# Optimization experiments

Hardware: AMD Instinct MI355X
Metric: run time of the kernel (lower is better)

## Reference

```python
import jax, jax.numpy as jnp
import numpy as np

N_INP = 10
N_REC = 200
ALPHA = 0.1          # dt / tau = 0.01 / 0.1
NOISE_STD = 0.01
W_REC_SCALE = 0.5
W_INP_SCALE = 0.1
BATCH = 256
T = 1000


def setup_inputs() -> dict:
    key = jax.random.key(0)
    kx, kwi, kwr = jax.random.split(key, 3)
    x = jax.random.normal(kx, (BATCH, T, N_INP), dtype=jnp.float32)
    h0 = jnp.zeros((BATCH, N_REC), dtype=jnp.float32)
    W_inp = (W_INP_SCALE / np.sqrt(N_INP)) * jax.random.normal(kwi, (N_REC, N_INP), dtype=jnp.float32)
    W_rec = (W_REC_SCALE / np.sqrt(N_REC)) * jax.random.normal(kwr, (N_REC, N_REC), dtype=jnp.float32)
    b_rec = jnp.zeros((N_REC,), dtype=jnp.float32)
    return {"x": x, "h0": h0, "W_inp": W_inp, "W_rec": W_rec, "b_rec": b_rec}


def reference(x, h0, W_inp, W_rec, b_rec):
    """Euler-discretized rate RNN: h' = h + alpha*(-h + tanh(W_rec h + W_inp x + b) + noise).
    Returns states: [batch, time, n_rec]."""
    B, Tlen, _ = x.shape
    # Precompute input drive for all timesteps in one GEMM: [B,T,n_rec]
    inp_term = jnp.einsum('bti,ri->btr', x, W_inp) + b_rec
    # Per-step noise, deterministic key (mirrors torch.randn_like each step)
    noise_key = jax.random.key(42)
    eta = NOISE_STD * jax.random.normal(noise_key, (Tlen, B, W_rec.shape[0]), dtype=x.dtype)

    def step(h, xs):
        inp_t, eta_t = xs
        preact = h @ W_rec.T + inp_t          # [B, n_rec]
        rate = jnp.tanh(preact)
        h_next = h + ALPHA * (-h + rate + eta_t)
        return h_next, h_next

    _, states = jax.lax.scan(step, h0, (jnp.swapaxes(inp_term, 0, 1), eta))
    return jnp.swapaxes(states, 0, 1)  # [B, T, n_rec]
```

## Files before the change

kernel.cpp:

```cpp
#include <hip/hip_runtime.h>
#include <cstdint>
#include <cstddef>

#define TSTEPS 1000
#define NB     256
#define NR     200
#define NI     10
#define ALPHA_F     0.1f
#define NOISE_STD_F 0.01f

__device__ __forceinline__ uint32_t rotl32(uint32_t v, uint32_t d) {
  return (v << d) | (v >> (32u - d));
}

__device__ __forceinline__ uint32_t threefry_bits(uint32_t c1) {
  const uint32_t ks0 = 0u;
  const uint32_t ks1 = 42u;
  const uint32_t ks2 = 0x1BD11BDAu ^ ks0 ^ ks1;
  uint32_t x0 = ks0;
  uint32_t x1 = c1 + ks1;
#define TFR(r) { x0 += x1; x1 = rotl32(x1, (r)); x1 ^= x0; }
  TFR(13) TFR(15) TFR(26) TFR(6)   x0 += ks1; x1 += ks2 + 1u;
  TFR(17) TFR(29) TFR(16) TFR(24)  x0 += ks2; x1 += ks0 + 2u;
  TFR(13) TFR(15) TFR(26) TFR(6)   x0 += ks0; x1 += ks1 + 3u;
  TFR(17) TFR(29) TFR(16) TFR(24)  x0 += ks1; x1 += ks2 + 4u;
  TFR(13) TFR(15) TFR(26) TFR(6)   x0 += ks2; x1 += ks0 + 5u;
#undef TFR
  return x0 ^ x1;
}

__device__ __forceinline__ float erfinv_f32(float x) {
  float w = -__logf(fmaf(-x, x, 1.0f));
  float p;
  if (w < 5.0f) {
    w = w - 2.5f;
    p = 2.81022636e-08f;
    p = fmaf(p, w, 3.43273939e-07f);
    p = fmaf(p, w, -3.5233877e-06f);
    p = fmaf(p, w, -4.39150654e-06f);
    p = fmaf(p, w, 0.00021858087f);
    p = fmaf(p, w, -0.00125372503f);
    p = fmaf(p, w, -0.00417768164f);
    p = fmaf(p, w, 0.246640727f);
    p = fmaf(p, w, 1.50140941f);
  } else {
    w = sqrtf(w) - 3.0f;
    p = -0.000200214257f;
    p = fmaf(p, w, 0.000100950558f);
    p = fmaf(p, w, 0.00134934322f);
    p = fmaf(p, w, -0.00367342844f);
    p = fmaf(p, w, 0.00573950773f);
    p = fmaf(p, w, -0.0076224613f);
    p = fmaf(p, w, 0.00943887047f);
    p = fmaf(p, w, 1.00167406f);
    p = fmaf(p, w, 2.83297682f);
  }
  return p * x;
}

__device__ __forceinline__ float jax_normal(uint32_t idx) {
  uint32_t bits = threefry_bits(idx);
  float f = __uint_as_float((bits >> 9) | 0x3F800000u) - 1.0f;
  const float lo = -0.99999994f;
  float u = fmaf(f, 2.0f, lo);
  u = fmaxf(lo, u);
  return 1.41421356f * erfinv_f32(u);
}

__device__ __forceinline__ float tanh_fast(float y) {
  float ay = fabsf(y);
  float t  = __expf(-2.0f * ay);
  float r  = (1.0f - t) * __frcp_rn(1.0f + t);
  return copysignf(r, y);
}

__device__ __forceinline__ void wg_barrier_lds() {
  asm volatile("s_waitcnt lgkmcnt(0)\n\ts_barrier" ::: "memory");
}

template <int CUR, bool PF>
__device__ __forceinline__ void rnn_step(
    int t, int tid, bool mac_active,
    const float (&w)[4][20], const float (&winp)[NI], float brec_r,
    float& h_reg, float*& obp, float& xnA, float& xnB,
    const float* __restrict__ xb, uint32_t nb_b,
    const float* __restrict__ hp, float* __restrict__ part_wp,
    float* __restrict__ sh_h, float* __restrict__ sh_part,
    float (*__restrict__ sh_x)[16], float (*__restrict__ sh_eta)[NR]) {
  constexpr int NXT = CUR ^ 1;

  if (mac_active) {
    float a0 = 0.0f, a1 = 0.0f, a2 = 0.0f, a3 = 0.0f;
#pragma unroll
    for (int q = 0; q < 5; ++q) {
      float4 hv = *(const float4*)(hp + 4 * q);
      a0 = fmaf(w[0][4 * q + 0], hv.x, a0);
      a1 = fmaf(w[1][4 * q + 0], hv.x, a1);
      a2 = fmaf(w[2][4 * q + 0], hv.x, a2);
      a3 = fmaf(w[3][4 * q + 0], hv.x, a3);
      a0 = fmaf(w[0][4 * q + 1], hv.y, a0);
      a1 = fmaf(w[1][4 * q + 1], hv.y, a1);
      a2 = fmaf(w[2][4 * q + 1], hv.y, a2);
      a3 = fmaf(w[3][4 * q + 1], hv.y, a3);
      a0 = fmaf(w[0][4 * q + 2], hv.z, a0);
      a1 = fmaf(w[1][4 * q + 2], hv.z, a1);
      a2 = fmaf(w[2][4 * q + 2], hv.z, a2);
      a3 = fmaf(w[3][4 * q + 2], hv.z, a3);
      a0 = fmaf(w[0][4 * q + 3], hv.w, a0);
      a1 = fmaf(w[1][4 * q + 3], hv.w, a1);
      a2 = fmaf(w[2][4 * q + 3], hv.w, a2);
      a3 = fmaf(w[3][4 * q + 3], hv.w, a3);
    }
    *(float4*)part_wp = make_float4(a0, a1, a2, a3);
  }
  wg_barrier_lds();

  if (tid < NR) {
    float y = brec_r;
#pragma unroll
    for (int q = 0; q < 10; ++q) y += sh_part[q * NR + tid];
    float4 xv0 = *(const float4*)(&sh_x[CUR][0]);
    float4 xv1 = *(const float4*)(&sh_x[CUR][4]);
    float2 xv2 = *(const float2*)(&sh_x[CUR][8]);
    y = fmaf(winp[0], xv0.x, y);
    y = fmaf(winp[1], xv0.y, y);
    y = fmaf(winp[2], xv0.z, y);
    y = fmaf(winp[3], xv0.w, y);
    y = fmaf(winp[4], xv1.x, y);
    y = fmaf(winp[5], xv1.y, y);
    y = fmaf(winp[6], xv1.z, y);
    y = fmaf(winp[7], xv1.w, y);
    y = fmaf(winp[8], xv2.x, y);
    y = fmaf(winp[9], xv2.y, y);
    float rate = tanh_fast(y);
    float eta  = sh_eta[CUR][tid];
    float hn = h_reg + ALPHA_F * (((-h_reg) + rate) + eta);
    h_reg = hn;
    sh_h[tid] = hn;
    *obp = hn;
    obp += NR;
  } else if ((tid >= 256 && tid < 448) || (tid < 208)) {
    if (PF) {
      int n = (tid >= 256) ? (tid - 256) : (tid - 8);
      uint32_t idx = (uint32_t)(t + 1) * (uint32_t)(NB * NR) + nb_b + (uint32_t)n;
      sh_eta[NXT][n] = NOISE_STD_F * jax_normal(idx);
    }
  } else if (tid >= 448 && tid < 448 + NI) {
    if (PF) {
      int j = tid - 448;
      sh_x[NXT][j] = (CUR == 0) ? xnA : xnB;
      int tf = t + 3;
      if (tf > TSTEPS - 1) tf = TSTEPS - 1;
      float xl = xb[tf * NI + j];
      if (CUR == 0) xnA = xl; else xnB = xl;
    }
  }
  wg_barrier_lds();
}

__launch_bounds__(512, 2)
__global__ void rnn_persistent(const float* __restrict__ x,
                               const float* __restrict__ h0,
                               const float* __restrict__ Winp,
                               const float* __restrict__ Wrec,
                               const float* __restrict__ brec,
                               float* __restrict__ out) {
  const int b   = blockIdx.x;
  const int tid = threadIdx.x;

  __shared__ float sh_h[NR];
  __shared__ float sh_part[10 * NR];
  __shared__ float sh_x[2][16];
  __shared__ float sh_eta[2][NR];

  const int  k_th = tid / 50;
  const int  r_th = tid % 50;
  const bool mac_active = (tid < 500);

  float w[4][20];
  if (mac_active) {
#pragma unroll
    for (int j = 0; j < 4; ++j) {
      const float* wr = Wrec + (size_t)(4 * r_th + j) * NR + 20 * k_th;
#pragma unroll
      for (int q = 0; q < 5; ++q) {
        float4 v = *(const float4*)(wr + 4 * q);
        w[j][4 * q + 0] = v.x; w[j][4 * q + 1] = v.y;
        w[j][4 * q + 2] = v.z; w[j][4 * q + 3] = v.w;
      }
    }
  }

  float winp[NI];
  float brec_r = 0.0f;
  float h_reg  = 0.0f;
  float* obp   = nullptr;

  const float* xb = x + (size_t)b * TSTEPS * NI;
  float* ob       = out + (size_t)b * TSTEPS * NR;

  if (tid < NR) {
#pragma unroll
    for (int i = 0; i < NI; ++i) winp[i] = Winp[tid * NI + i];
    brec_r = brec[tid];
    h_reg  = h0[(size_t)b * NR + tid];
    sh_h[tid] = h_reg;
    obp = ob + tid;
  }

  const uint32_t nb_b = (uint32_t)b * (uint32_t)NR;
  float xnA = 0.0f, xnB = 0.0f;

  if ((tid >= 256 && tid < 448) || (tid >= 200 && tid < 208)) {
    int n = (tid >= 256) ? (tid - 256) : (tid - 8);
    sh_eta[0][n] = NOISE_STD_F * jax_normal(nb_b + (uint32_t)n);
  } else if (tid >= 448 && tid < 448 + NI) {
    int j = tid - 448;
    sh_x[0][j] = xb[j];
    xnA = xb[NI + j];
    xnB = xb[2 * NI + j];
  }
  __syncthreads();

  const float* hp      = sh_h + 20 * k_th;
  float*       part_wp = sh_part + k_th * NR + 4 * r_th;

  for (int t = 0; t < TSTEPS - 2; t += 2) {
    rnn_step<0, true>(t,     tid, mac_active, w, winp, brec_r, h_reg, obp,
                      xnA, xnB, xb, nb_b, hp, part_wp,
                      sh_h, sh_part, sh_x, sh_eta);
    rnn_step<1, true>(t + 1, tid, mac_active, w, winp, brec_r, h_reg, obp,
                      xnA, xnB, xb, nb_b, hp, part_wp,
                      sh_h, sh_part, sh_x, sh_eta);
  }
  rnn_step<0, true >(TSTEPS - 2, tid, mac_active, w, winp, brec_r, h_reg, obp,
                     xnA, xnB, xb, nb_b, hp, part_wp,
                     sh_h, sh_part, sh_x, sh_eta);
  rnn_step<1, false>(TSTEPS - 1, tid, mac_active, w, winp, brec_r, h_reg, obp,
                     xnA, xnB, xb, nb_b, hp, part_wp,
                     sh_h, sh_part, sh_x, sh_eta);
}

extern "C" void kernel_launch(void* const* d_in, const int* in_sizes, int n_in,
                              void* d_out, int out_size, void* d_ws, size_t ws_size,
                              hipStream_t stream) {
  const float* x    = (const float*)d_in[0];
  const float* h0   = (const float*)d_in[1];
  const float* Winp = (const float*)d_in[2];
  const float* Wrec = (const float*)d_in[3];
  const float* brec = (const float*)d_in[4];
  float* out = (float*)d_out;
  (void)in_sizes; (void)n_in; (void)out_size; (void)d_ws; (void)ws_size;

  rnn_persistent<<<dim3(NB), dim3(512), 0, stream>>>(x, h0, Winp, Wrec, brec, out);
}
```

Baseline: 982.1 us.

## Give each thread a full W_rec row and use one barrier per step

Each of 200 active threads now keeps a whole W_rec row in registers and computes its dot product against a double-buffered shared h. This removes the cross-thread partial-sum reduction through shared memory and the second workgroup barrier in every timestep. Noise generation moves into the row threads and is held in registers one step ahead. The block shrinks to 256 threads. The trade-off is a longer serial FMA chain and RNG work per thread on the critical path, plus higher register pressure.

```diff
diff --git a/kernel.cpp b/kernel.cpp
--- a/kernel.cpp
+++ b/kernel.cpp
@@ -80,45 +80,53 @@
 
 template <int CUR, bool PF>
 __device__ __forceinline__ void rnn_step(
-    int t, int tid, bool mac_active,
-    const float (&w)[4][20], const float (&winp)[NI], float brec_r,
-    float& h_reg, float*& obp, float& xnA, float& xnB,
-    const float* __restrict__ xb, uint32_t nb_b,
-    const float* __restrict__ hp, float* __restrict__ part_wp,
-    float* __restrict__ sh_h, float* __restrict__ sh_part,
-    float (*__restrict__ sh_x)[16], float (*__restrict__ sh_eta)[NR]) {
+    int t, int row, bool row_active, bool xpipe, int jx,
+    const float (&w)[NR], const float (&winp)[NI], float brec_r,
+    float& h_reg, float& eta_use, float& eta_fill,
+    float& xnA, float& xnB, float*& obp,
+    const float* __restrict__ xb, uint32_t nbase,
+    float (&sh_h)[2][NR], float (&sh_x)[2][16]) {
   constexpr int NXT = CUR ^ 1;
 
-  if (mac_active) {
-    float a0 = 0.0f, a1 = 0.0f, a2 = 0.0f, a3 = 0.0f;
+  if (row_active) {
+    if (PF) {
+      uint32_t idx = (uint32_t)(t + 1) * (uint32_t)(NB * NR) + nbase;
+      eta_fill = NOISE_STD_F * jax_normal(idx);
+    }
+
+    float y = brec_r;
+    const float* hb = &sh_h[CUR][0];
 #pragma unroll
-    for (int q = 0; q < 5; ++q) {
-      float4 hv = *(const float4*)(hp + 4 * q);
-      a0 = fmaf(w[0][4 * q + 0], hv.x, a0);
-      a1 = fmaf(w[1][4 * q + 0], hv.x, a1);
-      a2 = fmaf(w[2][4 * q + 0], hv.x, a2);
-      a3 = fmaf(w[3][4 * q + 0], hv.x, a3);
-      a0 = fmaf(w[0][4 * q + 1], hv.y, a0);
-      a1 = fmaf(w[1][4 * q + 1], hv.y, a1);
-      a2 = fmaf(w[2][4 * q + 1], hv.y, a2);
-      a3 = fmaf(w[3][4 * q + 1], hv.y, a3);
-      a0 = fmaf(w[0][4 * q + 2], hv.z, a0);
-      a1 = fmaf(w[1][4 * q + 2], hv.z, a1);
-      a2 = fmaf(w[2][4 * q + 2], hv.z, a2);
-      a3 = fmaf(w[3][4 * q + 2], hv.z, a3);
-      a0 = fmaf(w[0][4 * q + 3], hv.w, a0);
-      a1 = fmaf(w[1][4 * q + 3], hv.w, a1);
-      a2 = fmaf(w[2][4 * q + 3], hv.w, a2);
-      a3 = fmaf(w[3][4 * q + 3], hv.w, a3);
-    }
-    *(float4*)part_wp = make_float4(a0, a1, a2, a3);
-  }
-  wg_barrier_lds();
-
-  if (tid < NR) {
-    float y = brec_r;
-#pragma unroll
-    for (int q = 0; q < 10; ++q) y += sh_part[q * NR + tid];
+    for (int q = 0; q < 10; ++q) {
+      float4 h0 = *(const float4*)(hb + 20 * q + 0);
+      float4 h1 = *(const float4*)(hb + 20 * q + 4);
+      float4 h2 = *(const float4*)(hb + 20 * q + 8);
+      float4 h3 = *(const float4*)(hb + 20 * q + 12);
+      float4 h4 = *(const float4*)(hb + 20 * q + 16);
+      float p = 0.0f;
+      p = fmaf(w[20 * q +  0], h0.x, p);
+      p = fmaf(w[20 * q +  1], h0.y, p);
+      p = fmaf(w[20 * q +  2], h0.z, p);
+      p = fmaf(w[20 * q +  3], h0.w, p);
+      p = fmaf(w[20 * q +  4], h1.x, p);
+      p = fmaf(w[20 * q +  5], h1.y, p);
+      p = fmaf(w[20 * q +  6], h1.z, p);
+      p = fmaf(w[20 * q +  7], h1.w, p);
+      p = fmaf(w[20 * q +  8], h2.x, p);
+      p = fmaf(w[20 * q +  9], h2.y, p);
+      p = fmaf(w[20 * q + 10], h2.z, p);
+      p = fmaf(w[20 * q + 11], h2.w, p);
+      p = fmaf(w[20 * q + 12], h3.x, p);
+      p = fmaf(w[20 * q + 13], h3.y, p);
+      p = fmaf(w[20 * q + 14], h3.z, p);
+      p = fmaf(w[20 * q + 15], h3.w, p);
+      p = fmaf(w[20 * q + 16], h4.x, p);
+      p = fmaf(w[20 * q + 17], h4.y, p);
+      p = fmaf(w[20 * q + 18], h4.z, p);
+      p = fmaf(w[20 * q + 19], h4.w, p);
+      y += p;
+    }
+
     float4 xv0 = *(const float4*)(&sh_x[CUR][0]);
     float4 xv1 = *(const float4*)(&sh_x[CUR][4]);
     float2 xv2 = *(const float2*)(&sh_x[CUR][8]);
@@ -132,33 +140,26 @@
     y = fmaf(winp[7], xv1.w, y);
     y = fmaf(winp[8], xv2.x, y);
     y = fmaf(winp[9], xv2.y, y);
+
     float rate = tanh_fast(y);
-    float eta  = sh_eta[CUR][tid];
-    float hn = h_reg + ALPHA_F * (((-h_reg) + rate) + eta);
+    float hn = h_reg + ALPHA_F * (((-h_reg) + rate) + eta_use);
     h_reg = hn;
-    sh_h[tid] = hn;
+    sh_h[NXT][row] = hn;
     *obp = hn;
     obp += NR;
-  } else if ((tid >= 256 && tid < 448) || (tid < 208)) {
+  } else if (xpipe) {
     if (PF) {
-      int n = (tid >= 256) ? (tid - 256) : (tid - 8);
-      uint32_t idx = (uint32_t)(t + 1) * (uint32_t)(NB * NR) + nb_b + (uint32_t)n;
-      sh_eta[NXT][n] = NOISE_STD_F * jax_normal(idx);
-    }
-  } else if (tid >= 448 && tid < 448 + NI) {
-    if (PF) {
-      int j = tid - 448;
-      sh_x[NXT][j] = (CUR == 0) ? xnA : xnB;
+      sh_x[NXT][jx] = (CUR == 0) ? xnA : xnB;
       int tf = t + 3;
       if (tf > TSTEPS - 1) tf = TSTEPS - 1;
-      float xl = xb[tf * NI + j];
+      float xl = xb[tf * NI + jx];
       if (CUR == 0) xnA = xl; else xnB = xl;
     }
   }
   wg_barrier_lds();
 }
 
-__launch_bounds__(512, 2)
+__launch_bounds__(256, 1)
 __global__ void rnn_persistent(const float* __restrict__ x,
                                const float* __restrict__ h0,
                                const float* __restrict__ Winp,
@@ -167,78 +168,66 @@
                                float* __restrict__ out) {
   const int b   = blockIdx.x;
   const int tid = threadIdx.x;
-
-  __shared__ float sh_h[NR];
-  __shared__ float sh_part[10 * NR];
+  const int wv  = tid >> 6;
+  const int ln  = tid & 63;
+
+  __shared__ float sh_h[2][NR];
   __shared__ float sh_x[2][16];
-  __shared__ float sh_eta[2][NR];
-
-  const int  k_th = tid / 50;
-  const int  r_th = tid % 50;
-  const bool mac_active = (tid < 500);
-
-  float w[4][20];
-  if (mac_active) {
-#pragma unroll
-    for (int j = 0; j < 4; ++j) {
-      const float* wr = Wrec + (size_t)(4 * r_th + j) * NR + 20 * k_th;
-#pragma unroll
-      for (int q = 0; q < 5; ++q) {
-        float4 v = *(const float4*)(wr + 4 * q);
-        w[j][4 * q + 0] = v.x; w[j][4 * q + 1] = v.y;
-        w[j][4 * q + 2] = v.z; w[j][4 * q + 3] = v.w;
-      }
-    }
-  }
-
+
+  const bool row_active = (ln < 50);
+  const int  row        = wv * 50 + ln;
+  const bool xpipe      = (tid >= 50 && tid < 50 + NI);
+  const int  jx         = tid - 50;
+
+  const float* xb = x + (size_t)b * TSTEPS * NI;
+  float* ob       = out + (size_t)b * TSTEPS * NR;
+
+  float w[NR];
   float winp[NI];
   float brec_r = 0.0f;
   float h_reg  = 0.0f;
-  float* obp   = nullptr;
-
-  const float* xb = x + (size_t)b * TSTEPS * NI;
-  float* ob       = out + (size_t)b * TSTEPS * NR;
-
-  if (tid < NR) {
+  float etaA = 0.0f, etaB = 0.0f;
+  float* obp = nullptr;
+  uint32_t nbase = 0;
+
+  if (row_active) {
+    const float* wr = Wrec + (size_t)row * NR;
 #pragma unroll
-    for (int i = 0; i < NI; ++i) winp[i] = Winp[tid * NI + i];
-    brec_r = brec[tid];
-    h_reg  = h0[(size_t)b * NR + tid];
-    sh_h[tid] = h_reg;
-    obp = ob + tid;
-  }
-
-  const uint32_t nb_b = (uint32_t)b * (uint32_t)NR;
+    for (int i = 0; i < 50; ++i) {
+      float4 v = *(const float4*)(wr + 4 * i);
+      w[4 * i + 0] = v.x; w[4 * i + 1] = v.y;
+      w[4 * i + 2] = v.z; w[4 * i + 3] = v.w;
+    }
+#pragma unroll
+    for (int i = 0; i < NI; ++i) winp[i] = Winp[row * NI + i];
+    brec_r = brec[row];
+    h_reg  = h0[(size_t)b * NR + row];
+    sh_h[0][row] = h_reg;
+    obp = ob + row;
+    nbase = (uint32_t)b * (uint32_t)NR + (uint32_t)row;
+    etaA = NOISE_STD_F * jax_normal(nbase);
+  } else if (xpipe) {
+    sh_x[0][jx] = xb[jx];
+    etaA = xb[NI + jx];
+    xnA_init:;
+  }
   float xnA = 0.0f, xnB = 0.0f;
-
-  if ((tid >= 256 && tid < 448) || (tid >= 200 && tid < 208)) {
-    int n = (tid >= 256) ? (tid - 256) : (tid - 8);
-    sh_eta[0][n] = NOISE_STD_F * jax_normal(nb_b + (uint32_t)n);
-  } else if (tid >= 448 && tid < 448 + NI) {
-    int j = tid - 448;
-    sh_x[0][j] = xb[j];
-    xnA = xb[NI + j];
-    xnB = xb[2 * NI + j];
+  if (xpipe) {
+    xnA = xb[NI + jx];
+    xnB = xb[2 * NI + jx];
   }
   __syncthreads();
 
-  const float* hp      = sh_h + 20 * k_th;
-  float*       part_wp = sh_part + k_th * NR + 4 * r_th;
-
   for (int t = 0; t < TSTEPS - 2; t += 2) {
-    rnn_step<0, true>(t,     tid, mac_active, w, winp, brec_r, h_reg, obp,
-                      xnA, xnB, xb, nb_b, hp, part_wp,
-                      sh_h, sh_part, sh_x, sh_eta);
-    rnn_step<1, true>(t + 1, tid, mac_active, w, winp, brec_r, h_reg, obp,
-                      xnA, xnB, xb, nb_b, hp, part_wp,
-                      sh_h, sh_part, sh_x, sh_eta);
-  }
-  rnn_step<0, true >(TSTEPS - 2, tid, mac_active, w, winp, brec_r, h_reg, obp,
-                     xnA, xnB, xb, nb_b, hp, part_wp,
-                     sh_h, sh_part, sh_x, sh_eta);
-  rnn_step<1, false>(TSTEPS - 1, tid, mac_active, w, winp, brec_r, h_reg, obp,
-                     xnA, xnB, xb, nb_b, hp, part_wp,
-                     sh_h, sh_part, sh_x, sh_eta);
+    rnn_step<0, true>(t,     row, row_active, xpipe, jx, w, winp, brec_r,
+                      h_reg, etaA, etaB, xnA, xnB, obp, xb, nbase, sh_h, sh_x);
+    rnn_step<1, true>(t + 1, row, row_active, xpipe, jx, w, winp, brec_r,
+                      h_reg, etaB, etaA, xnA, xnB, obp, xb, nbase, sh_h, sh_x);
+  }
+  rnn_step<0, true >(TSTEPS - 2, row, row_active, xpipe, jx, w, winp, brec_r,
+                     h_reg, etaA, etaB, xnA, xnB, obp, xb, nbase, sh_h, sh_x);
+  rnn_step<1, false>(TSTEPS - 1, row, row_active, xpipe, jx, w, winp, brec_r,
+                     h_reg, etaB, etaA, xnA, xnB, obp, xb, nbase, sh_h, sh_x);
 }
 
 extern "C" void kernel_launch(void* const* d_in, const int* in_sizes, int n_in,
@@ -252,5 +241,5 @@
   float* out = (float*)d_out;
   (void)in_sizes; (void)n_in; (void)out_size; (void)d_ws; (void)ws_size;
 
-  rnn_persistent<<<dim3(NB), dim3(512), 0, stream>>>(x, h0, Winp, Wrec, brec, out);
-}
+  rnn_persistent<<<dim3(NB), dim3(256), 0, stream>>>(x, h0, Winp, Wrec, brec, out);
+}
```

After: 1.498 ms. 1.53x slower.

## Precompute noise in a separate kernel and stream it into the RNN loop

Applied to the files above, without the earlier changes.

Adds a grid-wide noise_fill kernel that writes all Threefry/erfinv normal samples (about 205 MB) into the workspace. The persistent RNN kernel then prefetches each step's noise as float4 loads three steps ahead, instead of computing the RNG inside the serial step loop. The aim is to move RNG arithmetic off the latency-bound recurrence. The cost is a large extra global write and read pass, and the old in-loop path is kept as a fallback when the workspace is too small.

```diff
diff --git a/kernel.cpp b/kernel.cpp
--- a/kernel.cpp
+++ b/kernel.cpp
@@ -8,6 +8,8 @@
 #define NI     10
 #define ALPHA_F     0.1f
 #define NOISE_STD_F 0.01f
+#define ETA_STRIDE  (NB * NR)
+#define ETA_FLOATS  ((size_t)TSTEPS * NB * NR)
 
 __device__ __forceinline__ uint32_t rotl32(uint32_t v, uint32_t d) {
   return (v << d) | (v >> (32u - d));
@@ -78,12 +80,30 @@
   asm volatile("s_waitcnt lgkmcnt(0)\n\ts_barrier" ::: "memory");
 }
 
-template <int CUR, bool PF>
+__launch_bounds__(256)
+__global__ void noise_fill(float* __restrict__ ws) {
+  const int64_t nq = (int64_t)ETA_FLOATS / 4;
+  const int64_t stride = (int64_t)gridDim.x * blockDim.x;
+  for (int64_t i = (int64_t)blockIdx.x * blockDim.x + threadIdx.x;
+       i < nq; i += stride) {
+    uint32_t base = (uint32_t)(i * 4);
+    float4 v;
+    v.x = NOISE_STD_F * jax_normal(base + 0u);
+    v.y = NOISE_STD_F * jax_normal(base + 1u);
+    v.z = NOISE_STD_F * jax_normal(base + 2u);
+    v.w = NOISE_STD_F * jax_normal(base + 3u);
+    ((float4*)ws)[i] = v;
+  }
+}
+
+template <int CUR, bool PF, bool PRE>
 __device__ __forceinline__ void rnn_step(
     int t, int tid, bool mac_active,
     const float (&w)[4][20], const float (&winp)[NI], float brec_r,
     float& h_reg, float*& obp, float& xnA, float& xnB,
-    const float* __restrict__ xb, uint32_t nb_b,
+    float4& enA, float4& enB,
+    const float* __restrict__ xb, const float* __restrict__ etab,
+    uint32_t nb_b,
     const float* __restrict__ hp, float* __restrict__ part_wp,
     float* __restrict__ sh_h, float* __restrict__ sh_part,
     float (*__restrict__ sh_x)[16], float (*__restrict__ sh_eta)[NR]) {
@@ -139,11 +159,21 @@
     sh_h[tid] = hn;
     *obp = hn;
     obp += NR;
-  } else if ((tid >= 256 && tid < 448) || (tid < 208)) {
+  } else if (PRE ? (tid >= 256 && tid < 256 + NR / 4)
+                 : ((tid >= 256 && tid < 448) || (tid < 208))) {
     if (PF) {
-      int n = (tid >= 256) ? (tid - 256) : (tid - 8);
-      uint32_t idx = (uint32_t)(t + 1) * (uint32_t)(NB * NR) + nb_b + (uint32_t)n;
-      sh_eta[NXT][n] = NOISE_STD_F * jax_normal(idx);
+      if constexpr (PRE) {
+        int j = tid - 256;
+        *(float4*)(&sh_eta[NXT][4 * j]) = (CUR == 0) ? enA : enB;
+        int tf = t + 3;
+        if (tf > TSTEPS - 1) tf = TSTEPS - 1;
+        float4 e = *(const float4*)(etab + (size_t)tf * ETA_STRIDE + 4 * j);
+        if (CUR == 0) enA = e; else enB = e;
+      } else {
+        int n = (tid >= 256) ? (tid - 256) : (tid - 8);
+        uint32_t idx = (uint32_t)(t + 1) * (uint32_t)(NB * NR) + nb_b + (uint32_t)n;
+        sh_eta[NXT][n] = NOISE_STD_F * jax_normal(idx);
+      }
     }
   } else if (tid >= 448 && tid < 448 + NI) {
     if (PF) {
@@ -158,13 +188,15 @@
   wg_barrier_lds();
 }
 
-__launch_bounds__(512, 2)
-__global__ void rnn_persistent(const float* __restrict__ x,
-                               const float* __restrict__ h0,
-                               const float* __restrict__ Winp,
-                               const float* __restrict__ Wrec,
-                               const float* __restrict__ brec,
-                               float* __restrict__ out) {
+template <bool PRE>
+__global__ __launch_bounds__(512, 2)
+void rnn_persistent(const float* __restrict__ x,
+                    const float* __restrict__ h0,
+                    const float* __restrict__ Winp,
+                    const float* __restrict__ Wrec,
+                    const float* __restrict__ brec,
+                    const float* __restrict__ eta_ws,
+                    float* __restrict__ out) {
   const int b   = blockIdx.x;
   const int tid = threadIdx.x;
 
@@ -196,8 +228,9 @@
   float h_reg  = 0.0f;
   float* obp   = nullptr;
 
-  const float* xb = x + (size_t)b * TSTEPS * NI;
-  float* ob       = out + (size_t)b * TSTEPS * NR;
+  const float* xb   = x + (size_t)b * TSTEPS * NI;
+  const float* etab = PRE ? (eta_ws + (size_t)b * NR) : nullptr;
+  float* ob         = out + (size_t)b * TSTEPS * NR;
 
   if (tid < NR) {
 #pragma unroll
@@ -209,12 +242,24 @@
   }
 
   const uint32_t nb_b = (uint32_t)b * (uint32_t)NR;
-  float xnA = 0.0f, xnB = 0.0f;
-
-  if ((tid >= 256 && tid < 448) || (tid >= 200 && tid < 208)) {
-    int n = (tid >= 256) ? (tid - 256) : (tid - 8);
-    sh_eta[0][n] = NOISE_STD_F * jax_normal(nb_b + (uint32_t)n);
-  } else if (tid >= 448 && tid < 448 + NI) {
+  float  xnA = 0.0f, xnB = 0.0f;
+  float4 enA = make_float4(0.f, 0.f, 0.f, 0.f);
+  float4 enB = make_float4(0.f, 0.f, 0.f, 0.f);
+
+  if constexpr (PRE) {
+    if (tid >= 256 && tid < 256 + NR / 4) {
+      int j = tid - 256;
+      *(float4*)(&sh_eta[0][4 * j]) = *(const float4*)(etab + 4 * j);
+      enA = *(const float4*)(etab + (size_t)1 * ETA_STRIDE + 4 * j);
+      enB = *(const float4*)(etab + (size_t)2 * ETA_STRIDE + 4 * j);
+    }
+  } else {
+    if ((tid >= 256 && tid < 448) || (tid >= 200 && tid < 208)) {
+      int n = (tid >= 256) ? (tid - 256) : (tid - 8);
+      sh_eta[0][n] = NOISE_STD_F * jax_normal(nb_b + (uint32_t)n);
+    }
+  }
+  if (tid >= 448 && tid < 448 + NI) {
     int j = tid - 448;
     sh_x[0][j] = xb[j];
     xnA = xb[NI + j];
@@ -226,19 +271,19 @@
   float*       part_wp = sh_part + k_th * NR + 4 * r_th;
 
   for (int t = 0; t < TSTEPS - 2; t += 2) {
-    rnn_step<0, true>(t,     tid, mac_active, w, winp, brec_r, h_reg, obp,
-                      xnA, xnB, xb, nb_b, hp, part_wp,
-                      sh_h, sh_part, sh_x, sh_eta);
-    rnn_step<1, true>(t + 1, tid, mac_active, w, winp, brec_r, h_reg, obp,
-                      xnA, xnB, xb, nb_b, hp, part_wp,
-                      sh_h, sh_part, sh_x, sh_eta);
-  }
-  rnn_step<0, true >(TSTEPS - 2, tid, mac_active, w, winp, brec_r, h_reg, obp,
-                     xnA, xnB, xb, nb_b, hp, part_wp,
-                     sh_h, sh_part, sh_x, sh_eta);
-  rnn_step<1, false>(TSTEPS - 1, tid, mac_active, w, winp, brec_r, h_reg, obp,
-                     xnA, xnB, xb, nb_b, hp, part_wp,
-                     sh_h, sh_part, sh_x, sh_eta);
+    rnn_step<0, true, PRE>(t,     tid, mac_active, w, winp, brec_r, h_reg, obp,
+                           xnA, xnB, enA, enB, xb, etab, nb_b, hp, part_wp,
+                           sh_h, sh_part, sh_x, sh_eta);
+    rnn_step<1, true, PRE>(t + 1, tid, mac_active, w, winp, brec_r, h_reg, obp,
+                           xnA, xnB, enA, enB, xb, etab, nb_b, hp, part_wp,
+                           sh_h, sh_part, sh_x, sh_eta);
+  }
+  rnn_step<0, true,  PRE>(TSTEPS - 2, tid, mac_active, w, winp, brec_r, h_reg, obp,
+                          xnA, xnB, enA, enB, xb, etab, nb_b, hp, part_wp,
+                          sh_h, sh_part, sh_x, sh_eta);
+  rnn_step<1, false, PRE>(TSTEPS - 1, tid, mac_active, w, winp, brec_r, h_reg, obp,
+                          xnA, xnB, enA, enB, xb, etab, nb_b, hp, part_wp,
+                          sh_h, sh_part, sh_x, sh_eta);
 }
 
 extern "C" void kernel_launch(void* const* d_in, const int* in_sizes, int n_in,
@@ -250,7 +295,15 @@
   const float* Wrec = (const float*)d_in[3];
   const float* brec = (const float*)d_in[4];
   float* out = (float*)d_out;
-  (void)in_sizes; (void)n_in; (void)out_size; (void)d_ws; (void)ws_size;
-
-  rnn_persistent<<<dim3(NB), dim3(512), 0, stream>>>(x, h0, Winp, Wrec, brec, out);
-}
+  (void)in_sizes; (void)n_in; (void)out_size;
+
+  const size_t eta_bytes = ETA_FLOATS * sizeof(float);
+  if (d_ws != nullptr && ws_size >= eta_bytes) {
+    noise_fill<<<dim3(4096), dim3(256), 0, stream>>>((float*)d_ws);
+    rnn_persistent<true><<<dim3(NB), dim3(512), 0, stream>>>(
+        x, h0, Winp, Wrec, brec, (const float*)d_ws, out);
+  } else {
+    rnn_persistent<false><<<dim3(NB), dim3(512), 0, stream>>>(
+        x, h0, Winp, Wrec, brec, nullptr, out);
+  }
+}
```

After: 885.7 us. -9.8%, faster.
